# Optimization experiments

Measured on AMD Instinct MI355X. Metric: run time of the kernel, lower is better.

## Reference

```python
import jax, jax.numpy as jnp
import numpy as np

N0, IN, H = 262144, 128, 32
N1, N2 = 131072, 65536
E0, E1 = 2097152, 1048576
EPS = 1e-12


def _sage_conv(x_src, x_tgt, src, tgt, n_tgt, wl, bl, wr):
    # mean-aggregate neighbor features: scatter-add then divide by counts
    msg = x_src[src]                                        # [E, F] gather
    agg = jax.ops.segment_sum(msg, tgt, num_segments=n_tgt) # [n_tgt, F]
    cnt = jax.ops.segment_sum(jnp.ones((src.shape[0],), x_src.dtype), tgt,
                              num_segments=n_tgt)
    mean = agg / jnp.maximum(cnt, 1.0)[:, None]
    out = mean @ wl.T + bl + x_tgt @ wr.T                   # lin_l(agg) + lin_r(root)
    # normalize=True -> L2 normalize rows
    norm = jnp.maximum(jnp.linalg.norm(out, axis=-1, keepdims=True), EPS)
    return out / norm


def setup_inputs() -> dict:
    key = jax.random.key(0)
    ks = jax.random.split(key, 10)
    s = 1.0 / np.sqrt(IN)
    sh = 1.0 / np.sqrt(H)
    return {
        "x": jax.random.normal(ks[0], (N0, IN), jnp.float32),
        "src0": jax.random.randint(ks[1], (E0,), 0, N0),
        "tgt0": jax.random.randint(ks[2], (E0,), 0, N1),
        "src1": jax.random.randint(ks[3], (E1,), 0, N1),
        "tgt1": jax.random.randint(ks[4], (E1,), 0, N2),
        "wl0": jax.random.normal(ks[5], (H, IN), jnp.float32) * s,
        "bl0": jnp.zeros((H,), jnp.float32),
        "wr0": jax.random.normal(ks[6], (H, IN), jnp.float32) * s,
        "wl1": jax.random.normal(ks[7], (H, H), jnp.float32) * sh,
        "bl1": jnp.zeros((H,), jnp.float32),
        "wr1": jax.random.normal(ks[8], (H, H), jnp.float32) * sh,
        "n1": N1,
        "n2": N2,
    }


def reference(x, src0, tgt0, src1, tgt1, wl0, bl0, wr0, wl1, bl1, wr1, n1, n2):
    # layer 0: bipartite (x[:N0] sources -> first n1 nodes are targets)
    h = _sage_conv(x, x[:n1], src0, tgt0, n1, wl0, bl0, wr0)
    h = jax.nn.relu(h)
    # layer 1 (last layer: no relu)
    out = _sage_conv(h, h[:n2], src1, tgt1, n2, wl1, bl1, wr1)
    return out
```

## Files before the change

### kernel.cpp

```cpp
#include <hip/hip_runtime.h>

#define N0c 262144
#define INc 128
#define Hc  32
#define N1c 131072
#define N2c 65536
#define E0c 2097152
#define E1c 1048576

__device__ __forceinline__ void fma4(float4& a, float s, const float4 w) {
    a.x = fmaf(s, w.x, a.x);
    a.y = fmaf(s, w.y, a.y);
    a.z = fmaf(s, w.z, a.z);
    a.w = fmaf(s, w.w, a.w);
}

__global__ __launch_bounds__(256) void lin0_one_kernel(
    const float* __restrict__ x, const float* __restrict__ w,
    float* __restrict__ out)
{
    __shared__ float xs[128 * 32];
    __shared__ float ws[32 * 32];
    const int t = threadIdx.x;
    const int rowBase = blockIdx.x * 128;
    const int cg = t & 7;
    const int rg = t >> 3;

    float4* xs4w = (float4*)xs;
    const float4* xs4 = (const float4*)xs;
    const float4* ws4 = (const float4*)ws;

    float4 acc[4];
#pragma unroll
    for (int i = 0; i < 4; ++i) acc[i] = make_float4(0.f, 0.f, 0.f, 0.f);

    for (int kc = 0; kc < 4; ++kc) {
        if (kc) __syncthreads();
#pragma unroll
        for (int i = 0; i < 4; ++i) {
            int idx = t + 256 * i;
            int row = idx >> 3, kq = idx & 7;
            float4 v = ((const float4*)x)[(rowBase + row) * 32 + kc * 8 + kq];
            xs4w[row * 8 + ((kq + (row >> 2)) & 7)] = v;
        }
#pragma unroll
        for (int i = 0; i < 4; ++i) {
            int idx = t + 256 * i;
            int kk = idx & 31, j = idx >> 5;
            int dst = kk * 32 + 4 * (((j >> 2) + kk) & 7) + (j & 3);
            ws[dst] = w[j * 128 + kc * 32 + kk];
        }
        __syncthreads();

#pragma unroll
        for (int kq = 0; kq < 8; ++kq) {
            float4 xv[4];
#pragma unroll
            for (int i = 0; i < 4; ++i)
                xv[i] = xs4[(4 * rg + i) * 8 + ((kq + rg) & 7)];
            const int kb = 4 * kq;
            float4 w0 = ws4[(kb + 0) * 8 + ((cg + kb + 0) & 7)];
            float4 w1 = ws4[(kb + 1) * 8 + ((cg + kb + 1) & 7)];
            float4 w2 = ws4[(kb + 2) * 8 + ((cg + kb + 2) & 7)];
            float4 w3 = ws4[(kb + 3) * 8 + ((cg + kb + 3) & 7)];
#pragma unroll
            for (int i = 0; i < 4; ++i) {
                fma4(acc[i], xv[i].x, w0);
                fma4(acc[i], xv[i].y, w1);
                fma4(acc[i], xv[i].z, w2);
                fma4(acc[i], xv[i].w, w3);
            }
        }
    }

#pragma unroll
    for (int i = 0; i < 4; ++i) {
        int r = rowBase + 4 * rg + i;
        ((float4*)out)[r * 8 + cg] = acc[i];
    }
}

__global__ __launch_bounds__(128) void lin1_kernel(
    const float* __restrict__ h, const float* __restrict__ wl,
    const float* __restrict__ wr, float* __restrict__ y, float* __restrict__ z)
{
    __shared__ float xs[64 * 32];
    __shared__ float wls[32 * 32];
    __shared__ float wrs[32 * 32];
    const int t = threadIdx.x;
    const long rowBase = (long)blockIdx.x * 64;
    const bool doZ = rowBase < N2c;

#pragma unroll
    for (int i = 0; i < 8; ++i) {
        int idx = t + 128 * i;
        int j = idx >> 5, k = idx & 31;
        int dst = k * 32 + 4 * (((j >> 2) + k) & 7) + (j & 3);
        wls[dst] = wl[idx];
        if (doZ) wrs[dst] = wr[idx];
    }
#pragma unroll
    for (int i = 0; i < 4; ++i) {
        int idx = t + 128 * i;
        int row = idx >> 3, k4 = idx & 7;
        float4 v = ((const float4*)h)[rowBase * 8 + idx];
        ((float4*)xs)[row * 8 + ((k4 + (row >> 2)) & 7)] = v;
    }
    __syncthreads();

    const int cg = t & 7;
    const int rg = t >> 3;
    const float4* xs4  = (const float4*)xs;
    const float4* wls4 = (const float4*)wls;
    const float4* wrs4 = (const float4*)wrs;

    float4 accY[4], accZ[4];
#pragma unroll
    for (int i = 0; i < 4; ++i) {
        accY[i] = make_float4(0.f, 0.f, 0.f, 0.f);
        accZ[i] = make_float4(0.f, 0.f, 0.f, 0.f);
    }

#pragma unroll
    for (int k4 = 0; k4 < 8; ++k4) {
        float4 xv[4];
#pragma unroll
        for (int i = 0; i < 4; ++i)
            xv[i] = xs4[(4 * rg + i) * 8 + ((k4 + rg) & 7)];
        const int kb = 4 * k4;
        float4 w0 = wls4[(kb + 0) * 8 + ((cg + kb + 0) & 7)];
        float4 w1 = wls4[(kb + 1) * 8 + ((cg + kb + 1) & 7)];
        float4 w2 = wls4[(kb + 2) * 8 + ((cg + kb + 2) & 7)];
        float4 w3 = wls4[(kb + 3) * 8 + ((cg + kb + 3) & 7)];
#pragma unroll
        for (int i = 0; i < 4; ++i) {
            fma4(accY[i], xv[i].x, w0);
            fma4(accY[i], xv[i].y, w1);
            fma4(accY[i], xv[i].z, w2);
            fma4(accY[i], xv[i].w, w3);
        }
        if (doZ) {
            float4 u0 = wrs4[(kb + 0) * 8 + ((cg + kb + 0) & 7)];
            float4 u1 = wrs4[(kb + 1) * 8 + ((cg + kb + 1) & 7)];
            float4 u2 = wrs4[(kb + 2) * 8 + ((cg + kb + 2) & 7)];
            float4 u3 = wrs4[(kb + 3) * 8 + ((cg + kb + 3) & 7)];
#pragma unroll
            for (int i = 0; i < 4; ++i) {
                fma4(accZ[i], xv[i].x, u0);
                fma4(accZ[i], xv[i].y, u1);
                fma4(accZ[i], xv[i].z, u2);
                fma4(accZ[i], xv[i].w, u3);
            }
        }
    }
#pragma unroll
    for (int i = 0; i < 4; ++i) {
        long r = rowBase + 4 * rg + i;
        ((float4*)y)[r * 8 + cg] = accY[i];
        if (doZ) ((float4*)z)[r * 8 + cg] = accZ[i];
    }
}

__global__ __launch_bounds__(256) void bhist_kernel(
    const int* __restrict__ tgt, int* __restrict__ bcnt, int nb)
{
    __shared__ int hist[256];
    const int t = threadIdx.x;
    const int base = blockIdx.x * 8192;
    hist[t] = 0;
    __syncthreads();
#pragma unroll 4
    for (int i = 0; i < 32; ++i)
        atomicAdd(&hist[tgt[base + i * 256 + t] >> 9], 1);
    __syncthreads();
    if (t < nb && hist[t]) atomicAdd(&bcnt[t], hist[t]);
}

__global__ __launch_bounds__(256) void bscan_kernel(
    const int* __restrict__ bcnt, int* __restrict__ bbase,
    int* __restrict__ bcur, int nb, int nE)
{
    __shared__ int s[256];
    int t = threadIdx.x;
    int local = (t < nb) ? bcnt[t] : 0;
    s[t] = local;
    __syncthreads();
    int v = local;
#pragma unroll
    for (int off = 1; off < 256; off <<= 1) {
        int u = (t >= off) ? s[t - off] : 0;
        __syncthreads();
        v += u;
        s[t] = v;
        __syncthreads();
    }
    int ex = v - local;
    if (t < nb) {
        bbase[t] = ex;
        bcur[t] = ex;
    }
    if (t == nb - 1) bbase[nb] = nE;
}

__global__ __launch_bounds__(256) void part_kernel(
    const int* __restrict__ src, const int* __restrict__ tgt,
    int2* __restrict__ pairs, int* __restrict__ bcur, int nb)
{
    __shared__ int hist[256];
    __shared__ int bbase[256];
    const int t = threadIdx.x;
    const int base = blockIdx.x * 8192;
    hist[t] = 0;
    __syncthreads();
#pragma unroll 4
    for (int i = 0; i < 32; ++i) {
        int e = base + i * 256 + t;
        atomicAdd(&hist[tgt[e] >> 9], 1);
    }
    __syncthreads();
    if (t < nb) bbase[t] = atomicAdd(&bcur[t], hist[t]);
    __syncthreads();
    hist[t] = 0;
    __syncthreads();
#pragma unroll 4
    for (int i = 0; i < 32; ++i) {
        int e = base + i * 256 + t;
        int tv = tgt[e], sv = src[e];
        int b = tv >> 9;
        int r = atomicAdd(&hist[b], 1);
        pairs[bbase[b] + r] = make_int2(sv, tv);
    }
}

__global__ __launch_bounds__(512) void sortb_kernel(
    const int2* __restrict__ pairs, const int* __restrict__ bbase,
    int* __restrict__ cnt, int* __restrict__ cur, int* __restrict__ eidx)
{
    __shared__ int cl[512];
    __shared__ int offs[512];
    const int b = blockIdx.x;
    const int t = threadIdx.x;
    const int tlo = b << 9;
    const int beg = bbase[b];
    const int end = bbase[b + 1];

    cl[t] = 0;
    __syncthreads();
    for (int e = beg + t; e < end; e += 512)
        atomicAdd(&cl[pairs[e].y - tlo], 1);
    __syncthreads();
    int local = cl[t];
    offs[t] = local;
    __syncthreads();
    int v = local;
#pragma unroll
    for (int off = 1; off < 512; off <<= 1) {
        int u = (t >= off) ? offs[t - off] : 0;
        __syncthreads();
        v += u;
        offs[t] = v;
        __syncthreads();
    }
    int ex = v - local;
    cnt[tlo + t] = local;
    cur[tlo + t] = beg + ex;
    __syncthreads();
    offs[t] = beg + ex;
    cl[t] = 0;
    __syncthreads();
    for (int e = beg + t; e < end; e += 512) {
        int2 p = pairs[e];
        int li = p.y - tlo;
        int r = atomicAdd(&cl[li], 1);
        eidx[offs[li] + r] = p.x;
    }
}

__global__ __launch_bounds__(256) void gather_agg_kernel(
    const float* __restrict__ yv, const int* __restrict__ eidx,
    const int* __restrict__ cnt, const int* __restrict__ cur,
    const float* __restrict__ z, const float* __restrict__ b,
    float* __restrict__ out, int n, int doRelu)
{
    int t = blockIdx.x * 256 + threadIdx.x;
    int row = t >> 3, part = t & 7;
    if (row >= n) return;
    int c = cnt[row];
    int beg = cur[row];
    int end = beg + c;
    const float4* y4 = (const float4*)yv;
    float4 acc = make_float4(0.f, 0.f, 0.f, 0.f);
    int e = beg;
    for (; e + 1 < end; e += 2) {
        int s0 = eidx[e], s1 = eidx[e + 1];
        float4 v0 = y4[(long)s0 * 8 + part];
        float4 v1 = y4[(long)s1 * 8 + part];
        acc.x += v0.x + v1.x;
        acc.y += v0.y + v1.y;
        acc.z += v0.z + v1.z;
        acc.w += v0.w + v1.w;
    }
    if (e < end) {
        int s0 = eidx[e];
        float4 v0 = y4[(long)s0 * 8 + part];
        acc.x += v0.x; acc.y += v0.y; acc.z += v0.z; acc.w += v0.w;
    }
    float inv = 1.f / fmaxf((float)c, 1.f);
    float4 bb = ((const float4*)b)[part];
    float4 zz = ((const float4*)z)[(long)row * 8 + part];
    float4 v;
    v.x = fmaf(acc.x, inv, bb.x) + zz.x;
    v.y = fmaf(acc.y, inv, bb.y) + zz.y;
    v.z = fmaf(acc.z, inv, bb.z) + zz.z;
    v.w = fmaf(acc.w, inv, bb.w) + zz.w;
    float ss = v.x * v.x + v.y * v.y + v.z * v.z + v.w * v.w;
    ss += __shfl_xor(ss, 1);
    ss += __shfl_xor(ss, 2);
    ss += __shfl_xor(ss, 4);
    float q = 1.f / fmaxf(sqrtf(ss), 1e-12f);
    v.x *= q; v.y *= q; v.z *= q; v.w *= q;
    if (doRelu) {
        v.x = fmaxf(v.x, 0.f); v.y = fmaxf(v.y, 0.f);
        v.z = fmaxf(v.z, 0.f); v.w = fmaxf(v.w, 0.f);
    }
    ((float4*)out)[(long)row * 8 + part] = v;
}

extern "C" void kernel_launch(void* const* d_in, const int* in_sizes, int n_in,
                              void* d_out, int out_size, void* d_ws, size_t ws_size,
                              hipStream_t stream) {
    const float* x   = (const float*)d_in[0];
    const int* src0  = (const int*)d_in[1];
    const int* tgt0  = (const int*)d_in[2];
    const int* src1  = (const int*)d_in[3];
    const int* tgt1  = (const int*)d_in[4];
    const float* wl0 = (const float*)d_in[5];
    const float* bl0 = (const float*)d_in[6];
    const float* wr0 = (const float*)d_in[7];
    const float* wl1 = (const float*)d_in[8];
    const float* bl1 = (const float*)d_in[9];
    const float* wr1 = (const float*)d_in[10];

    char* W = (char*)d_ws;
    float* y0    = (float*)(W + 0);
    float* y1    = (float*)(W + 0);
    float* z1    = (float*)(W + 16777216);
    int*   eidx1 = (int*)  (W + 25165824);
    int*   cnt1  = (int*)  (W + 29360128);
    int*   cur1  = (int*)  (W + 29622272);
    float* z0    = (float*)(W + 33554432);
    int2*  pairs1= (int2*) (W + 33554432);
    int2*  pairs0= (int2*) (W + 50331648);
    float* h     = (float*)(W + 50331648);
    int*   eidx0 = (int*)  (W + 67108864);
    int*   cnt0  = (int*)  (W + 75497472);
    int*   cur0  = (int*)  (W + 76021760);
    int*   bcnt  = (int*)  (W + 76546048);
    int*   bbase = (int*)  (W + 76547072);
    int*   bcur  = (int*)  (W + 76549120);

    hipMemsetAsync(bcnt, 0, 1024, stream);
    lin0_one_kernel<<<N0c / 128, 256, 0, stream>>>(x, wl0, y0);
    lin0_one_kernel<<<N1c / 128, 256, 0, stream>>>(x, wr0, z0);
    bhist_kernel<<<E0c / 8192, 256, 0, stream>>>(tgt0, bcnt, 256);
    bscan_kernel<<<1, 256, 0, stream>>>(bcnt, bbase, bcur, 256, E0c);
    part_kernel<<<E0c / 8192, 256, 0, stream>>>(src0, tgt0, pairs0, bcur, 256);
    sortb_kernel<<<N1c / 512, 512, 0, stream>>>(pairs0, bbase, cnt0, cur0, eidx0);
    gather_agg_kernel<<<(N1c * 8) / 256, 256, 0, stream>>>(y0, eidx0, cnt0, cur0,
                                                           z0, bl0, h, N1c, 1);

    hipMemsetAsync(bcnt, 0, 1024, stream);
    bhist_kernel<<<E1c / 8192, 256, 0, stream>>>(tgt1, bcnt, 128);
    bscan_kernel<<<1, 256, 0, stream>>>(bcnt, bbase, bcur, 128, E1c);
    part_kernel<<<E1c / 8192, 256, 0, stream>>>(src1, tgt1, pairs1, bcur, 128);
    lin1_kernel<<<N1c / 64, 128, 0, stream>>>(h, wl1, wr1, y1, z1);
    sortb_kernel<<<N2c / 512, 512, 0, stream>>>(pairs1, bbase, cnt1, cur1, eidx1);
    gather_agg_kernel<<<(N2c * 8) / 256, 256, 0, stream>>>(y1, eidx1, cnt1, cur1,
                                                           z1, bl1, (float*)d_out, N2c, 0);
}
```

Before: 465.4 us.

## Fuse bucket sort and gather into LDS-atomic bucket aggregation with bf16 messages

Measured after the change: 1.052 ms. 126% more time.

```diff
diff --git a/kernel.cpp b/kernel.cpp
--- a/kernel.cpp
+++ b/kernel.cpp
@@ -15,9 +15,20 @@
     a.w = fmaf(s, w.w, a.w);
 }
 
+__device__ __forceinline__ unsigned short f2bf(float f) {
+    unsigned u = __float_as_uint(f);
+    u += 0x7fffu + ((u >> 16) & 1u);
+    return (unsigned short)(u >> 16);
+}
+__device__ __forceinline__ ushort4 pack4(float4 v) {
+    return make_ushort4(f2bf(v.x), f2bf(v.y), f2bf(v.z), f2bf(v.w));
+}
+__device__ __forceinline__ float bflo(unsigned u) { return __uint_as_float(u << 16); }
+__device__ __forceinline__ float bfhi(unsigned u) { return __uint_as_float(u & 0xffff0000u); }
+
 __global__ __launch_bounds__(256) void lin0_one_kernel(
     const float* __restrict__ x, const float* __restrict__ w,
-    float* __restrict__ out)
+    unsigned short* __restrict__ outb, float* __restrict__ outf)
 {
     __shared__ float xs[128 * 32];
     __shared__ float ws[32 * 32];
@@ -73,16 +84,25 @@
         }
     }
 
-#pragma unroll
-    for (int i = 0; i < 4; ++i) {
-        int r = rowBase + 4 * rg + i;
-        ((float4*)out)[r * 8 + cg] = acc[i];
+    if (outb) {
+#pragma unroll
+        for (int i = 0; i < 4; ++i) {
+            int r = rowBase + 4 * rg + i;
+            ((ushort4*)outb)[r * 8 + cg] = pack4(acc[i]);
+        }
+    } else {
+#pragma unroll
+        for (int i = 0; i < 4; ++i) {
+            int r = rowBase + 4 * rg + i;
+            ((float4*)outf)[r * 8 + cg] = acc[i];
+        }
     }
 }
 
 __global__ __launch_bounds__(128) void lin1_kernel(
     const float* __restrict__ h, const float* __restrict__ wl,
-    const float* __restrict__ wr, float* __restrict__ y, float* __restrict__ z)
+    const float* __restrict__ wr, unsigned short* __restrict__ y,
+    float* __restrict__ z)
 {
     __shared__ float xs[64 * 32];
     __shared__ float wls[32 * 32];
@@ -156,7 +176,7 @@
 #pragma unroll
     for (int i = 0; i < 4; ++i) {
         long r = rowBase + 4 * rg + i;
-        ((float4*)y)[r * 8 + cg] = accY[i];
+        ((ushort4*)y)[r * 8 + cg] = pack4(accY[i]);
         if (doZ) ((float4*)z)[r * 8 + cg] = accZ[i];
     }
 }
@@ -232,98 +252,75 @@
     }
 }
 
-__global__ __launch_bounds__(512) void sortb_kernel(
+#define AGG_S 33
+__global__ __launch_bounds__(1024) void bucket_agg_kernel(
     const int2* __restrict__ pairs, const int* __restrict__ bbase,
-    int* __restrict__ cnt, int* __restrict__ cur, int* __restrict__ eidx)
-{
-    __shared__ int cl[512];
-    __shared__ int offs[512];
+    const unsigned short* __restrict__ y, const float* __restrict__ z,
+    const float* __restrict__ bias, float* __restrict__ out, int doRelu)
+{
+    __shared__ float agg[512 * AGG_S];
+    __shared__ int ccnt[512];
+    const int t = threadIdx.x;
     const int b = blockIdx.x;
-    const int t = threadIdx.x;
     const int tlo = b << 9;
     const int beg = bbase[b];
     const int end = bbase[b + 1];
 
-    cl[t] = 0;
-    __syncthreads();
-    for (int e = beg + t; e < end; e += 512)
-        atomicAdd(&cl[pairs[e].y - tlo], 1);
-    __syncthreads();
-    int local = cl[t];
-    offs[t] = local;
-    __syncthreads();
-    int v = local;
-#pragma unroll
-    for (int off = 1; off < 512; off <<= 1) {
-        int u = (t >= off) ? offs[t - off] : 0;
-        __syncthreads();
-        v += u;
-        offs[t] = v;
-        __syncthreads();
-    }
-    int ex = v - local;
-    cnt[tlo + t] = local;
-    cur[tlo + t] = beg + ex;
-    __syncthreads();
-    offs[t] = beg + ex;
-    cl[t] = 0;
-    __syncthreads();
-    for (int e = beg + t; e < end; e += 512) {
+    for (int i = t; i < 512 * AGG_S; i += 1024) agg[i] = 0.f;
+    if (t < 512) ccnt[t] = 0;
+    __syncthreads();
+
+    for (int e = beg + t; e < end; e += 1024) {
         int2 p = pairs[e];
         int li = p.y - tlo;
-        int r = atomicAdd(&cl[li], 1);
-        eidx[offs[li] + r] = p.x;
-    }
-}
-
-__global__ __launch_bounds__(256) void gather_agg_kernel(
-    const float* __restrict__ yv, const int* __restrict__ eidx,
-    const int* __restrict__ cnt, const int* __restrict__ cur,
-    const float* __restrict__ z, const float* __restrict__ b,
-    float* __restrict__ out, int n, int doRelu)
-{
-    int t = blockIdx.x * 256 + threadIdx.x;
-    int row = t >> 3, part = t & 7;
-    if (row >= n) return;
-    int c = cnt[row];
-    int beg = cur[row];
-    int end = beg + c;
-    const float4* y4 = (const float4*)yv;
-    float4 acc = make_float4(0.f, 0.f, 0.f, 0.f);
-    int e = beg;
-    for (; e + 1 < end; e += 2) {
-        int s0 = eidx[e], s1 = eidx[e + 1];
-        float4 v0 = y4[(long)s0 * 8 + part];
-        float4 v1 = y4[(long)s1 * 8 + part];
-        acc.x += v0.x + v1.x;
-        acc.y += v0.y + v1.y;
-        acc.z += v0.z + v1.z;
-        acc.w += v0.w + v1.w;
-    }
-    if (e < end) {
-        int s0 = eidx[e];
-        float4 v0 = y4[(long)s0 * 8 + part];
-        acc.x += v0.x; acc.y += v0.y; acc.z += v0.z; acc.w += v0.w;
-    }
-    float inv = 1.f / fmaxf((float)c, 1.f);
-    float4 bb = ((const float4*)b)[part];
-    float4 zz = ((const float4*)z)[(long)row * 8 + part];
-    float4 v;
-    v.x = fmaf(acc.x, inv, bb.x) + zz.x;
-    v.y = fmaf(acc.y, inv, bb.y) + zz.y;
-    v.z = fmaf(acc.z, inv, bb.z) + zz.z;
-    v.w = fmaf(acc.w, inv, bb.w) + zz.w;
-    float ss = v.x * v.x + v.y * v.y + v.z * v.z + v.w * v.w;
-    ss += __shfl_xor(ss, 1);
-    ss += __shfl_xor(ss, 2);
-    ss += __shfl_xor(ss, 4);
-    float q = 1.f / fmaxf(sqrtf(ss), 1e-12f);
-    v.x *= q; v.y *= q; v.z *= q; v.w *= q;
-    if (doRelu) {
-        v.x = fmaxf(v.x, 0.f); v.y = fmaxf(v.y, 0.f);
-        v.z = fmaxf(v.z, 0.f); v.w = fmaxf(v.w, 0.f);
-    }
-    ((float4*)out)[(long)row * 8 + part] = v;
+        atomicAdd(&ccnt[li], 1);
+        const uint4* yr = (const uint4*)(y + (long)p.x * 32);
+        float* ar = &agg[li * AGG_S];
+#pragma unroll
+        for (int j = 0; j < 4; ++j) {
+            uint4 q = yr[j];
+            float* a8 = ar + j * 8;
+            __hip_atomic_fetch_add(a8 + 0, bflo(q.x), __ATOMIC_RELAXED, __HIP_MEMORY_SCOPE_WORKGROUP);
+            __hip_atomic_fetch_add(a8 + 1, bfhi(q.x), __ATOMIC_RELAXED, __HIP_MEMORY_SCOPE_WORKGROUP);
+            __hip_atomic_fetch_add(a8 + 2, bflo(q.y), __ATOMIC_RELAXED, __HIP_MEMORY_SCOPE_WORKGROUP);
+            __hip_atomic_fetch_add(a8 + 3, bfhi(q.y), __ATOMIC_RELAXED, __HIP_MEMORY_SCOPE_WORKGROUP);
+            __hip_atomic_fetch_add(a8 + 4, bflo(q.z), __ATOMIC_RELAXED, __HIP_MEMORY_SCOPE_WORKGROUP);
+            __hip_atomic_fetch_add(a8 + 5, bfhi(q.z), __ATOMIC_RELAXED, __HIP_MEMORY_SCOPE_WORKGROUP);
+            __hip_atomic_fetch_add(a8 + 6, bflo(q.w), __ATOMIC_RELAXED, __HIP_MEMORY_SCOPE_WORKGROUP);
+            __hip_atomic_fetch_add(a8 + 7, bfhi(q.w), __ATOMIC_RELAXED, __HIP_MEMORY_SCOPE_WORKGROUP);
+        }
+    }
+    __syncthreads();
+
+    const int part = t & 7;
+    const int rloc = t >> 3;
+    const float4 bb = ((const float4*)bias)[part];
+    const float4* z4 = (const float4*)z;
+    float4* o4 = (float4*)out;
+#pragma unroll
+    for (int r0 = 0; r0 < 512; r0 += 128) {
+        int row = r0 + rloc;
+        long g = tlo + row;
+        float inv = 1.f / fmaxf((float)ccnt[row], 1.f);
+        const float* ar = &agg[row * AGG_S + part * 4];
+        float4 zz = z4[g * 8 + part];
+        float4 v;
+        v.x = fmaf(ar[0], inv, bb.x) + zz.x;
+        v.y = fmaf(ar[1], inv, bb.y) + zz.y;
+        v.z = fmaf(ar[2], inv, bb.z) + zz.z;
+        v.w = fmaf(ar[3], inv, bb.w) + zz.w;
+        float ss = v.x * v.x + v.y * v.y + v.z * v.z + v.w * v.w;
+        ss += __shfl_xor(ss, 1);
+        ss += __shfl_xor(ss, 2);
+        ss += __shfl_xor(ss, 4);
+        float q = 1.f / fmaxf(sqrtf(ss), 1e-12f);
+        v.x *= q; v.y *= q; v.z *= q; v.w *= q;
+        if (doRelu) {
+            v.x = fmaxf(v.x, 0.f); v.y = fmaxf(v.y, 0.f);
+            v.z = fmaxf(v.z, 0.f); v.w = fmaxf(v.w, 0.f);
+        }
+        o4[g * 8 + part] = v;
+    }
 }
 
 extern "C" void kernel_launch(void* const* d_in, const int* in_sizes, int n_in,
@@ -342,39 +339,30 @@
     const float* wr1 = (const float*)d_in[10];
 
     char* W = (char*)d_ws;
-    float* y0    = (float*)(W + 0);
-    float* y1    = (float*)(W + 0);
-    float* z1    = (float*)(W + 16777216);
-    int*   eidx1 = (int*)  (W + 25165824);
-    int*   cnt1  = (int*)  (W + 29360128);
-    int*   cur1  = (int*)  (W + 29622272);
-    float* z0    = (float*)(W + 33554432);
-    int2*  pairs1= (int2*) (W + 33554432);
-    int2*  pairs0= (int2*) (W + 50331648);
-    float* h     = (float*)(W + 50331648);
-    int*   eidx0 = (int*)  (W + 67108864);
-    int*   cnt0  = (int*)  (W + 75497472);
-    int*   cur0  = (int*)  (W + 76021760);
-    int*   bcnt  = (int*)  (W + 76546048);
-    int*   bbase = (int*)  (W + 76547072);
-    int*   bcur  = (int*)  (W + 76549120);
+    unsigned short* y0 = (unsigned short*)(W + 0);
+    float*  z0    = (float*) (W + 16777216);
+    int2*   pairs0= (int2*)  (W + 33554432);
+    float*  h     = (float*) (W + 50331648);
+    unsigned short* y1 = (unsigned short*)(W + 67108864);
+    float*  z1    = (float*) (W + 75497472);
+    int2*   pairs1= (int2*)  (W + 83886080);
+    int*    bcnt  = (int*)   (W + 92274688);
+    int*    bbase = (int*)   (W + 92275712);
+    int*    bcur  = (int*)   (W + 92277760);
 
     hipMemsetAsync(bcnt, 0, 1024, stream);
-    lin0_one_kernel<<<N0c / 128, 256, 0, stream>>>(x, wl0, y0);
-    lin0_one_kernel<<<N1c / 128, 256, 0, stream>>>(x, wr0, z0);
+    lin0_one_kernel<<<N0c / 128, 256, 0, stream>>>(x, wl0, y0, nullptr);
+    lin0_one_kernel<<<N1c / 128, 256, 0, stream>>>(x, wr0, nullptr, z0);
     bhist_kernel<<<E0c / 8192, 256, 0, stream>>>(tgt0, bcnt, 256);
     bscan_kernel<<<1, 256, 0, stream>>>(bcnt, bbase, bcur, 256, E0c);
     part_kernel<<<E0c / 8192, 256, 0, stream>>>(src0, tgt0, pairs0, bcur, 256);
-    sortb_kernel<<<N1c / 512, 512, 0, stream>>>(pairs0, bbase, cnt0, cur0, eidx0);
-    gather_agg_kernel<<<(N1c * 8) / 256, 256, 0, stream>>>(y0, eidx0, cnt0, cur0,
-                                                           z0, bl0, h, N1c, 1);
+    bucket_agg_kernel<<<256, 1024, 0, stream>>>(pairs0, bbase, y0, z0, bl0, h, 1);
 
     hipMemsetAsync(bcnt, 0, 1024, stream);
     bhist_kernel<<<E1c / 8192, 256, 0, stream>>>(tgt1, bcnt, 128);
     bscan_kernel<<<1, 256, 0, stream>>>(bcnt, bbase, bcur, 128, E1c);
     part_kernel<<<E1c / 8192, 256, 0, stream>>>(src1, tgt1, pairs1, bcur, 128);
     lin1_kernel<<<N1c / 64, 128, 0, stream>>>(h, wl1, wr1, y1, z1);
-    sortb_kernel<<<N2c / 512, 512, 0, stream>>>(pairs1, bbase, cnt1, cur1, eidx1);
-    gather_agg_kernel<<<(N2c * 8) / 256, 256, 0, stream>>>(y1, eidx1, cnt1, cur1,
-                                                           z1, bl1, (float*)d_out, N2c, 0);
-}
+    bucket_agg_kernel<<<128, 1024, 0, stream>>>(pairs1, bbase, y1, z1, bl1,
+                                                (float*)d_out, 0);
+}
```
